# Kernel tuning notes

Measured on AMD Instinct MI355X. Metric: run time of the kernel, lower is better.

The kernel has to match this reference:

```python
import jax, jax.numpy as jnp
import numpy as np

B, n, A = 64, 1024, 32          # graphs, nodes/graph, actions/graph
N = B * n
EH = 2048                        # undirected edges per graph
HID, H = 128, 4
C = HID // H
NF, EF, AD, NI, L = 1, 1, 7, 4, 3
NEG_SLOPE = 0.2


def setup_inputs() -> dict:
    ks = jax.random.split(jax.random.key(0), 16)
    x = jax.random.normal(ks[0], (N, NF), jnp.float32)
    s = jax.random.randint(ks[1], (B, EH), 0, n)
    d = jax.random.randint(ks[2], (B, EH), 0, n)
    off = (jnp.arange(B) * n)[:, None]
    s = (s + off).reshape(-1)
    d = (d + off).reshape(-1)
    # bidirectional edges (unrooted trees): both i->j and j->i
    edge_index = jnp.stack([jnp.concatenate([s, d]), jnp.concatenate([d, s])]).astype(jnp.int32)
    E = edge_index.shape[1]
    edge_attr = jax.random.uniform(ks[3], (E, EF), jnp.float32)
    idx = jax.random.randint(ks[4], (B, A, NI), 0, n).astype(jnp.float32)
    meta = jax.random.normal(ks[5], (B, A, AD - NI), jnp.float32)
    action_tensor = jnp.concatenate([idx, meta], axis=-1)
    batch_idx = jnp.repeat(jnp.arange(B, dtype=jnp.int32), n)
    batch_ptr = jnp.arange(B + 1, dtype=jnp.int32) * n

    def lin(k, i, o):
        return jax.random.normal(k, (i, o), jnp.float32) / np.float32(np.sqrt(i))

    inp = dict(x=x, edge_attr=edge_attr, action_tensor=action_tensor,
               edge_index=edge_index, batch_idx=batch_idx, batch_ptr=batch_ptr)
    inp["Wn"] = lin(ks[6], NF, HID); inp["bn"] = jnp.zeros((HID,), jnp.float32)
    kl = jax.random.split(ks[7], 4 * L)
    inp["gWl"] = jnp.stack([lin(kl[i], HID, HID) for i in range(L)])
    inp["gWr"] = jnp.stack([lin(kl[L + i], HID, HID) for i in range(L)])
    inp["gWe"] = jnp.stack([lin(kl[2 * L + i], EF, HID) for i in range(L)])
    inp["gatt"] = jnp.stack([jax.random.normal(kl[3 * L + i], (H, C), jnp.float32) * 0.1 for i in range(L)])
    inp["gbl"] = jnp.zeros((L, HID), jnp.float32)
    inp["gbr"] = jnp.zeros((L, HID), jnp.float32)
    inp["gb"] = jnp.zeros((L, HID), jnp.float32)
    mlp_in = NI * HID + (AD - NI)
    inp["aW1"] = lin(ks[8], mlp_in, HID); inp["ab1"] = jnp.zeros((HID,), jnp.float32)
    inp["aW2"] = lin(ks[9], HID, HID); inp["ab2"] = jnp.zeros((HID,), jnp.float32)
    inp["qW1"] = lin(ks[10], 4 * HID, HID); inp["qb1"] = jnp.zeros((HID,), jnp.float32)
    inp["qW2"] = lin(ks[11], HID, HID); inp["qb2"] = jnp.zeros((HID,), jnp.float32)
    inp["qW3"] = lin(ks[12], HID, 1); inp["qb3"] = jnp.zeros((1,), jnp.float32)
    return inp


def _gatv2(h, src, dst, ea, Wl, bl, Wr, br, We, att, b):
    # PyG GATv2Conv: e_ij = att . leaky_relu(lin_l(x_j) + lin_r(x_i) + lin_edge(e_ij))
    Nn = h.shape[0]
    xl = (h @ Wl + bl).reshape(Nn, H, C)   # source transform
    xr = (h @ Wr + br).reshape(Nn, H, C)   # target transform
    ee = (ea @ We).reshape(-1, H, C)       # edge transform (no bias in PyG)
    e = jax.nn.leaky_relu(xl[src] + xr[dst] + ee, NEG_SLOPE)   # [E,H,C]
    logits = jnp.einsum('ehc,hc->eh', e, att)
    m = jax.ops.segment_max(logits, dst, num_segments=Nn)       # stable softmax per target node
    ex = jnp.exp(logits - m[dst])
    alpha = ex / jax.ops.segment_sum(ex, dst, num_segments=Nn)[dst]
    msg = (xl[src] * alpha[:, :, None]).reshape(-1, HID)
    return jax.ops.segment_sum(msg, dst, num_segments=Nn) + b


def reference(x, edge_attr, action_tensor, Wn, bn, gWl, gbl, gWr, gbr, gWe, gatt, gb,
              aW1, ab1, aW2, ab2, qW1, qb1, qW2, qb2, qW3, qb3,
              edge_index, batch_idx, batch_ptr):
    Nn = x.shape[0]
    nb = batch_ptr.shape[0] - 1
    # GATv2Conv default add_self_loops=True, fill_value='mean' for edge_attr
    loops = jnp.arange(Nn, dtype=edge_index.dtype)
    src = jnp.concatenate([edge_index[0], loops])
    dst = jnp.concatenate([edge_index[1], loops])
    ea = jnp.concatenate([edge_attr, jnp.broadcast_to(edge_attr.mean(0), (Nn, edge_attr.shape[1]))], 0)
    h = jax.nn.relu(x @ Wn + bn)
    for l in range(L):
        h = jax.nn.relu(_gatv2(h, src, dst, ea, gWl[l], gbl[l], gWr[l], gbr[l], gWe[l], gatt[l], gb[l])) + h
    # sum / mean / max pooling per graph
    sums = jax.ops.segment_sum(h, batch_idx, num_segments=nb)
    cnt = jax.ops.segment_sum(jnp.ones((Nn, 1), h.dtype), batch_idx, num_segments=nb)
    means = sums / cnt
    maxs = jax.ops.segment_max(h, batch_idx, num_segments=nb)
    tree_emb = jnp.concatenate([sums, means, maxs], -1)          # [B, 3*HID]
    # action encoding: gather node embeddings at action node indices (shifted by batch_ptr)
    ni = action_tensor[..., :NI].astype(jnp.int32) + batch_ptr[:-1][:, None, None]
    g = h[ni].reshape(nb, action_tensor.shape[1], NI * HID)
    ai = jnp.concatenate([g, action_tensor[..., NI:]], -1)
    ae = jax.nn.relu(jax.nn.relu(ai @ aW1 + ab1) @ aW2 + ab2)    # [B, A, HID]
    comb = jnp.concatenate([jnp.broadcast_to(tree_emb[:, None, :], (nb, ae.shape[1], 3 * HID)), ae], -1)
    q = jax.nn.relu(comb @ qW1 + qb1)
    q = jax.nn.relu(q @ qW2 + qb2)
    return (q @ qW3 + qb3).squeeze(-1)                            # [B, A]
```

## Files before the change

### kernel.cpp

```cpp
#include <hip/hip_runtime.h>
#include <hip/hip_bf16.h>

#define NNODES 65536
#define NGRAPH 64
#define NPG 1024
#define NACT 32
#define HID 128
#define DEGS 32

typedef __attribute__((ext_vector_type(8))) short bf16x8;
typedef __attribute__((ext_vector_type(4))) float f32x4;

__device__ __forceinline__ void load8(float* dst, const float* src) {
    float4 q0 = ((const float4*)src)[0];
    float4 q1 = ((const float4*)src)[1];
    dst[0]=q0.x; dst[1]=q0.y; dst[2]=q0.z; dst[3]=q0.w;
    dst[4]=q1.x; dst[5]=q1.y; dst[6]=q1.z; dst[7]=q1.w;
}

__device__ __forceinline__ void load8bf(float* dst, const unsigned short* src) {
    uint4 q = *(const uint4*)src;
    dst[0] = __uint_as_float(q.x << 16); dst[1] = __uint_as_float(q.x & 0xffff0000u);
    dst[2] = __uint_as_float(q.y << 16); dst[3] = __uint_as_float(q.y & 0xffff0000u);
    dst[4] = __uint_as_float(q.z << 16); dst[5] = __uint_as_float(q.z & 0xffff0000u);
    dst[6] = __uint_as_float(q.w << 16); dst[7] = __uint_as_float(q.w & 0xffff0000u);
}

__device__ __forceinline__ unsigned short f2bf(float f) {
    unsigned int u = __float_as_uint(f);
    u = (u + 0x7fffu + ((u >> 16) & 1u)) >> 16;
    return (unsigned short)u;
}

__global__ void setup_k(const int* __restrict__ ei, const float* __restrict__ ea,
                        int* __restrict__ cursor, float* __restrict__ meansum,
                        int2* __restrict__ csr, int E0, int nsb,
                        const float* __restrict__ gWl, const float* __restrict__ gWr,
                        unsigned short* __restrict__ wtl, unsigned short* __restrict__ wtr,
                        const float* __restrict__ aW1, const float* __restrict__ aW2,
                        const float* __restrict__ qW1, const float* __restrict__ qW2,
                        unsigned short* __restrict__ wA1t, unsigned short* __restrict__ wA2t,
                        unsigned short* __restrict__ wQ1t, unsigned short* __restrict__ wQ2t) {
    int bid = blockIdx.x, t = threadIdx.x;
    if (bid < nsb) {
        __shared__ float s[256];
        int e = bid * 256 + t;
        float v = 0.f;
        if (e < E0) {
            int sn = ei[e], d = ei[E0 + e];
            int pos = atomicAdd(&cursor[d], 1);
            if (pos >= DEGS) pos = DEGS - 1;
            csr[(size_t)d * DEGS + pos] = make_int2(sn, __float_as_int(ea[e]));
            v = ea[e];
        }
        s[t] = v; __syncthreads();
        for (int off = 128; off > 0; off >>= 1) { if (t < off) s[t] += s[t+off]; __syncthreads(); }
        if (t == 0) atomicAdd(meansum, s[0]);
    } else if (bid < nsb + 192) {
        int idx = (bid - nsb) * 256 + t;
        int l = idx >> 14, rem = idx & 16383;
        int n = rem >> 7, k = rem & 127;
        int src = l*16384 + k*128 + n;
        wtl[idx] = f2bf(gWl[src]);
        wtr[idx] = f2bf(gWr[src]);
    } else {
        int n = bid - nsb - 192;
        for (int k = t; k < 544; k += 256)
            wA1t[n*544 + k] = (k < 515) ? f2bf(aW1[(size_t)k*128 + n]) : (unsigned short)0;
        if (t < 128) {
            wA2t[n*128 + t] = f2bf(aW2[(size_t)t*128 + n]);
            wQ1t[n*128 + t] = f2bf(qW1[(size_t)(384 + t)*128 + n]);
            wQ2t[n*128 + t] = f2bf(qW2[(size_t)t*128 + n]);
        }
    }
}

__global__ __launch_bounds__(256) void gemm_lr_mfma_k(
    const unsigned short* __restrict__ hb, const float* __restrict__ x,
    const float* __restrict__ Wn, const float* __restrict__ bn, int l0,
    const unsigned short* __restrict__ wtl, const unsigned short* __restrict__ wtr,
    const float* __restrict__ bl, const float* __restrict__ br,
    unsigned short* __restrict__ xlb, unsigned short* __restrict__ xrb) {
    int wave = threadIdx.x >> 6;
    int lane = threadIdx.x & 63;
    int lr = lane & 15;
    int lq = lane >> 4;
    int r0 = blockIdx.x * 128 + wave * 32;

    bf16x8 a[2][4];
    if (l0) {
        float xv0 = x[r0 + lr], xv1 = x[r0 + 16 + lr];
#pragma unroll
        for (int kf = 0; kf < 4; ++kf) {
            float wn[8], bv[8];
            load8(wn, Wn + kf*32 + lq*8);
            load8(bv, bn + kf*32 + lq*8);
            union { bf16x8 v; unsigned short u[8]; } p0, p1;
#pragma unroll
            for (int j = 0; j < 8; ++j) {
                p0.u[j] = f2bf(fmaxf(fmaf(xv0, wn[j], bv[j]), 0.f));
                p1.u[j] = f2bf(fmaxf(fmaf(xv1, wn[j], bv[j]), 0.f));
            }
            a[0][kf] = p0.v; a[1][kf] = p1.v;
        }
    } else {
        const short* hs = (const short*)hb;
#pragma unroll
        for (int rt = 0; rt < 2; ++rt)
#pragma unroll
            for (int kf = 0; kf < 4; ++kf)
                a[rt][kf] = *(const bf16x8*)(hs + (size_t)(r0 + rt*16 + lr)*HID + kf*32 + lq*8);
    }

    const short* ws[2]   = {(const short*)wtl, (const short*)wtr};
    const float* bias[2] = {bl, br};
    unsigned short* outp[2] = {xlb, xrb};

#pragma unroll
    for (int m = 0; m < 2; ++m) {
        const short* W = ws[m];
        f32x4 acc[2][8];
#pragma unroll
        for (int rt = 0; rt < 2; ++rt)
#pragma unroll
            for (int ct = 0; ct < 8; ++ct) acc[rt][ct] = (f32x4){0.f,0.f,0.f,0.f};

        bf16x8 b[4], nb2[4];
#pragma unroll
        for (int kf = 0; kf < 4; ++kf)
            b[kf] = *(const bf16x8*)(W + (size_t)(lr)*HID + kf*32 + lq*8);
#pragma unroll
        for (int ct = 0; ct < 8; ++ct) {
            if (ct < 7) {
#pragma unroll
                for (int kf = 0; kf < 4; ++kf)
                    nb2[kf] = *(const bf16x8*)(W + (size_t)((ct+1)*16 + lr)*HID + kf*32 + lq*8);
            }
#pragma unroll
            for (int rt = 0; rt < 2; ++rt)
#pragma unroll
                for (int kf = 0; kf < 4; ++kf)
                    acc[rt][ct] = __builtin_amdgcn_mfma_f32_16x16x32_bf16(a[rt][kf], b[kf], acc[rt][ct], 0, 0, 0);
#pragma unroll
            for (int kf = 0; kf < 4; ++kf) b[kf] = nb2[kf];
        }
#pragma unroll
        for (int ct = 0; ct < 8; ++ct) {
            float bv = bias[m][ct*16 + lr];
#pragma unroll
            for (int rt = 0; rt < 2; ++rt)
#pragma unroll
                for (int rg = 0; rg < 4; ++rg) {
                    int row = r0 + rt*16 + lq*4 + rg;
                    outp[m][(size_t)row*HID + ct*16 + lr] = f2bf(acc[rt][ct][rg] + bv);
                }
        }
    }
}

__global__ __launch_bounds__(256, 4) void gat_edge_k(
    const unsigned short* __restrict__ xlb, const unsigned short* __restrict__ xrb,
    unsigned short* __restrict__ hb,
    const int* __restrict__ deg, const int2* __restrict__ csr,
    const float* __restrict__ We, const float* __restrict__ att,
    const float* __restrict__ gb, const float* __restrict__ meansum, float inv_e0,
    const float* __restrict__ x, const float* __restrict__ Wn, const float* __restrict__ bn,
    int l0, int do_pool, float* __restrict__ tree_sum, float* __restrict__ tree_max) {
    __shared__ float ps[16][132];
    __shared__ float pm[16][132];
    int xcd  = blockIdx.x & 7;
    int slot = blockIdx.x >> 3;
    int g    = xcd * 8 + (slot >> 6);
    int j    = slot & 63;
    int t    = threadIdx.x;
    int nd   = t >> 4;
    int v    = g * NPG + j * 16 + nd;
    int li   = t & 15;
    int base = li * 8;
    float mea = meansum[0] * inv_e0;

    float xrv[8], attv[8], wev[8];
    load8bf(xrv, xrb + (size_t)v*HID + base);
    load8(attv, att + base);
    load8(wev, We + base);

    float acc[8], xs0[8];
    load8bf(xs0, xlb + (size_t)v*HID + base);
    float m;
    {
        float lg = 0.f;
#pragma unroll
        for (int c = 0; c < 8; ++c) {
            float e = xs0[c] + xrv[c] + mea * wev[c];
            e = fmaxf(e, 0.2f * e);
            lg = fmaf(attv[c], e, lg);
        }
        lg += __shfl_xor(lg, 1, 64);
        lg += __shfl_xor(lg, 2, 64);
        m = lg;
#pragma unroll
        for (int c = 0; c < 8; ++c) acc[c] = xs0[c];
    }
    float den = 1.f;

    int dg = deg[v];
    if (dg > DEGS) dg = DEGS;
    const int2* cp = csr + (size_t)v * DEGS;
    for (int i0 = 0; i0 < dg; i0 += 4) {
        int nch = dg - i0; if (nch > 4) nch = 4;
        int2 ee[4];
        float xs[4][8];
#pragma unroll
        for (int u = 0; u < 4; ++u)
            ee[u] = cp[i0 + ((u < nch) ? u : nch - 1)];
#pragma unroll
        for (int u = 0; u < 4; ++u)
            load8bf(xs[u], xlb + (size_t)ee[u].x*HID + base);
#pragma unroll
        for (int u = 0; u < 4; ++u) {
            if (u < nch) {
                float an = __int_as_float(ee[u].y);
                float lg = 0.f;
#pragma unroll
                for (int c = 0; c < 8; ++c) {
                    float e = xs[u][c] + xrv[c] + an * wev[c];
                    e = fmaxf(e, 0.2f * e);
                    lg = fmaf(attv[c], e, lg);
                }
                lg += __shfl_xor(lg, 1, 64);
                lg += __shfl_xor(lg, 2, 64);
                float mn  = fmaxf(m, lg);
                float sc  = __expf(m - mn);
                float wgt = __expf(lg - mn);
                den = den * sc + wgt;
#pragma unroll
                for (int c = 0; c < 8; ++c) acc[c] = acc[c] * sc + wgt * xs[u][c];
                m = mn;
            }
        }
    }

    float inv = 1.f / den;
    size_t o = (size_t)v*HID + base;
    float hold[8], gbv[8];
    if (l0) {
        float xv = x[v];
        float wn[8], bv[8];
        load8(wn, Wn + base);
        load8(bv, bn + base);
#pragma unroll
        for (int c = 0; c < 8; ++c) hold[c] = fmaxf(fmaf(xv, wn[c], bv[c]), 0.f);
    } else {
        load8bf(hold, hb + o);
    }
    load8(gbv, gb + base);
    float nh[8];
#pragma unroll
    for (int c = 0; c < 8; ++c) {
        float val = acc[c] * inv + gbv[c];
        val = val > 0.f ? val : 0.f;
        nh[c] = val + hold[c];
    }
    unsigned int* hbp = (unsigned int*)(hb + o);
#pragma unroll
    for (int q = 0; q < 4; ++q)
        hbp[q] = (unsigned int)f2bf(nh[2*q]) | ((unsigned int)f2bf(nh[2*q+1]) << 16);

    if (do_pool) {
#pragma unroll
        for (int c = 0; c < 8; ++c) { ps[nd][base + c] = nh[c]; pm[nd][base + c] = nh[c]; }
        __syncthreads();
        if (t < 128) {
            float s = 0.f;
#pragma unroll
            for (int n = 0; n < 16; ++n) s += ps[n][t];
            atomicAdd(&tree_sum[g*128 + t], s);
        } else {
            int col = t - 128;
            float mx = 0.f;
#pragma unroll
            for (int n = 0; n < 16; ++n) mx = fmaxf(mx, pm[n][col]);
            atomicMax((int*)&tree_max[g*128 + col], __float_as_int(mx));
        }
    }
}

#define SA1 552
#define SAC 136
__global__ __launch_bounds__(256) void action_q_k(
    const unsigned short* __restrict__ hb, const float* __restrict__ action,
    const int* __restrict__ batch_ptr,
    const float* __restrict__ tree_sum, const float* __restrict__ tree_max,
    const unsigned short* __restrict__ wA1t, const float* __restrict__ ab1,
    const unsigned short* __restrict__ wA2t, const float* __restrict__ ab2,
    const float* __restrict__ qW1, const unsigned short* __restrict__ wQ1t,
    const float* __restrict__ qb1,
    const unsigned short* __restrict__ wQ2t, const float* __restrict__ qb2,
    const float* __restrict__ qW3, const float* __restrict__ qb3,
    float* __restrict__ out) {
    int b = blockIdx.x;
    int t = threadIdx.x;
    int w  = t >> 6;
    int lane = t & 63;
    int lr = lane & 15;
    int lq = lane >> 4;

    __shared__ unsigned short aib[32 * SA1];
    __shared__ unsigned short z1s[32 * SAC];
    __shared__ unsigned short aes[32 * SAC];
    __shared__ unsigned short q1s[32 * SAC];
    __shared__ float q2f[32 * 132];
    __shared__ float tqA[128], tqB[128];
    __shared__ float psum[32][8];

    int ptr = batch_ptr[b];

    {
        int p = t >> 1, half = t & 1;
        int a = p >> 2, j = p & 3;
        const float* actp = action + (size_t)(b * NACT + a) * 7;
        int ni = (int)actp[j] + ptr;
        const uint4* src = (const uint4*)(hb + (size_t)ni * HID) + half * 8;
        uint4* dst = (uint4*)((char*)aib + ((size_t)a * SA1 + j * 128 + half * 64) * 2);
#pragma unroll
        for (int q = 0; q < 8; ++q) dst[q] = src[q];
        if (t < 32) {
            const float* ap = action + (size_t)(b * NACT + t) * 7;
            aib[t * SA1 + 512] = f2bf(ap[4]);
            aib[t * SA1 + 513] = f2bf(ap[5]);
            aib[t * SA1 + 514] = f2bf(ap[6]);
            for (int i = 3; i < 40; ++i) aib[t * SA1 + 512 + i] = 0;
        }
    }

    {
        if (t < 128) {
            int col = t;
            float acc = 0.f;
#pragma unroll 4
            for (int k = 0; k < 128; ++k) {
                float sv = tree_sum[b * 128 + k];
                acc = fmaf(sv, qW1[(size_t)k * 128 + col], acc);
                acc = fmaf(sv * (1.f / 1024.f), qW1[(size_t)(128 + k) * 128 + col], acc);
            }
            tqA[col] = acc;
        } else {
            int col = t - 128;
            float acc = 0.f;
#pragma unroll 4
            for (int k = 0; k < 128; ++k) {
                float mv = tree_max[b * 128 + k];
                acc = fmaf(mv, qW1[(size_t)(256 + k) * 128 + col], acc);
            }
            tqB[col] = acc;
        }
    }
    __syncthreads();

    f32x4 acc[2][2];
    const unsigned short* srcA;
    int strideA, K;

    srcA = aib; strideA = SA1; K = 544;
#pragma unroll
    for (int rt = 0; rt < 2; ++rt)
#pragma unroll
        for (int ci = 0; ci < 2; ++ci) acc[rt][ci] = (f32x4){0.f, 0.f, 0.f, 0.f};
    for (int ks = 0; ks < K; ks += 32) {
        bf16x8 a0 = *(const bf16x8*)(srcA + (0 * 16 + lr) * strideA + ks + lq * 8);
        bf16x8 a1 = *(const bf16x8*)(srcA + (1 * 16 + lr) * strideA + ks + lq * 8);
        bf16x8 b0 = *(const bf16x8*)(wA1t + (size_t)((2 * w + 0) * 16 + lr) * K + ks + lq * 8);
        bf16x8 b1 = *(const bf16x8*)(wA1t + (size_t)((2 * w + 1) * 16 + lr) * K + ks + lq * 8);
        acc[0][0] = __builtin_amdgcn_mfma_f32_16x16x32_bf16(a0, b0, acc[0][0], 0, 0, 0);
        acc[0][1] = __builtin_amdgcn_mfma_f32_16x16x32_bf16(a0, b1, acc[0][1], 0, 0, 0);
        acc[1][0] = __builtin_amdgcn_mfma_f32_16x16x32_bf16(a1, b0, acc[1][0], 0, 0, 0);
        acc[1][1] = __builtin_amdgcn_mfma_f32_16x16x32_bf16(a1, b1, acc[1][1], 0, 0, 0);
    }
#pragma unroll
    for (int ci = 0; ci < 2; ++ci) {
        int col = (2 * w + ci) * 16 + lr;
        float bv = ab1[col];
#pragma unroll
        for (int rt = 0; rt < 2; ++rt)
#pragma unroll
            for (int rg = 0; rg < 4; ++rg) {
                int row = rt * 16 + lq * 4 + rg;
                z1s[row * SAC + col] = f2bf(fmaxf(acc[rt][ci][rg] + bv, 0.f));
            }
    }
    __syncthreads();

    srcA = z1s; strideA = SAC; K = 128;
#pragma unroll
    for (int rt = 0; rt < 2; ++rt)
#pragma unroll
        for (int ci = 0; ci < 2; ++ci) acc[rt][ci] = (f32x4){0.f, 0.f, 0.f, 0.f};
#pragma unroll
    for (int ks = 0; ks < 128; ks += 32) {
        bf16x8 a0 = *(const bf16x8*)(srcA + (0 * 16 + lr) * strideA + ks + lq * 8);
        bf16x8 a1 = *(const bf16x8*)(srcA + (1 * 16 + lr) * strideA + ks + lq * 8);
        bf16x8 b0 = *(const bf16x8*)(wA2t + (size_t)((2 * w + 0) * 16 + lr) * K + ks + lq * 8);
        bf16x8 b1 = *(const bf16x8*)(wA2t + (size_t)((2 * w + 1) * 16 + lr) * K + ks + lq * 8);
        acc[0][0] = __builtin_amdgcn_mfma_f32_16x16x32_bf16(a0, b0, acc[0][0], 0, 0, 0);
        acc[0][1] = __builtin_amdgcn_mfma_f32_16x16x32_bf16(a0, b1, acc[0][1], 0, 0, 0);
        acc[1][0] = __builtin_amdgcn_mfma_f32_16x16x32_bf16(a1, b0, acc[1][0], 0, 0, 0);
        acc[1][1] = __builtin_amdgcn_mfma_f32_16x16x32_bf16(a1, b1, acc[1][1], 0, 0, 0);
    }
#pragma unroll
    for (int ci = 0; ci < 2; ++ci) {
        int col = (2 * w + ci) * 16 + lr;
        float bv = ab2[col];
#pragma unroll
        for (int rt = 0; rt < 2; ++rt)
#pragma unroll
            for (int rg = 0; rg < 4; ++rg) {
                int row = rt * 16 + lq * 4 + rg;
                aes[row * SAC + col] = f2bf(fmaxf(acc[rt][ci][rg] + bv, 0.f));
            }
    }
    __syncthreads();

    srcA = aes; strideA = SAC; K = 128;
#pragma unroll
    for (int rt = 0; rt < 2; ++rt)
#pragma unroll
        for (int ci = 0; ci < 2; ++ci) acc[rt][ci] = (f32x4){0.f, 0.f, 0.f, 0.f};
#pragma unroll
    for (int ks = 0; ks < 128; ks += 32) {
        bf16x8 a0 = *(const bf16x8*)(srcA + (0 * 16 + lr) * strideA + ks + lq * 8);
        bf16x8 a1 = *(const bf16x8*)(srcA + (1 * 16 + lr) * strideA + ks + lq * 8);
        bf16x8 b0 = *(const bf16x8*)(wQ1t + (size_t)((2 * w + 0) * 16 + lr) * K + ks + lq * 8);
        bf16x8 b1 = *(const bf16x8*)(wQ1t + (size_t)((2 * w + 1) * 16 + lr) * K + ks + lq * 8);
        acc[0][0] = __builtin_amdgcn_mfma_f32_16x16x32_bf16(a0, b0, acc[0][0], 0, 0, 0);
        acc[0][1] = __builtin_amdgcn_mfma_f32_16x16x32_bf16(a0, b1, acc[0][1], 0, 0, 0);
        acc[1][0] = __builtin_amdgcn_mfma_f32_16x16x32_bf16(a1, b0, acc[1][0], 0, 0, 0);
        acc[1][1] = __builtin_amdgcn_mfma_f32_16x16x32_bf16(a1, b1, acc[1][1], 0, 0, 0);
    }
#pragma unroll
    for (int ci = 0; ci < 2; ++ci) {
        int col = (2 * w + ci) * 16 + lr;
        float bv = qb1[col] + tqA[col] + tqB[col];
#pragma unroll
        for (int rt = 0; rt < 2; ++rt)
#pragma unroll
            for (int rg = 0; rg < 4; ++rg) {
                int row = rt * 16 + lq * 4 + rg;
                q1s[row * SAC + col] = f2bf(fmaxf(acc[rt][ci][rg] + bv, 0.f));
            }
    }
    __syncthreads();

    srcA = q1s; strideA = SAC; K = 128;
#pragma unroll
    for (int rt = 0; rt < 2; ++rt)
#pragma unroll
        for (int ci = 0; ci < 2; ++ci) acc[rt][ci] = (f32x4){0.f, 0.f, 0.f, 0.f};
#pragma unroll
    for (int ks = 0; ks < 128; ks += 32) {
        bf16x8 a0 = *(const bf16x8*)(srcA + (0 * 16 + lr) * strideA + ks + lq * 8);
        bf16x8 a1 = *(const bf16x8*)(srcA + (1 * 16 + lr) * strideA + ks + lq * 8);
        bf16x8 b0 = *(const bf16x8*)(wQ2t + (size_t)((2 * w + 0) * 16 + lr) * K + ks + lq * 8);
        bf16x8 b1 = *(const bf16x8*)(wQ2t + (size_t)((2 * w + 1) * 16 + lr) * K + ks + lq * 8);
        acc[0][0] = __builtin_amdgcn_mfma_f32_16x16x32_bf16(a0, b0, acc[0][0], 0, 0, 0);
        acc[0][1] = __builtin_amdgcn_mfma_f32_16x16x32_bf16(a0, b1, acc[0][1], 0, 0, 0);
        acc[1][0] = __builtin_amdgcn_mfma_f32_16x16x32_bf16(a1, b0, acc[1][0], 0, 0, 0);
        acc[1][1] = __builtin_amdgcn_mfma_f32_16x16x32_bf16(a1, b1, acc[1][1], 0, 0, 0);
    }
#pragma unroll
    for (int ci = 0; ci < 2; ++ci) {
        int col = (2 * w + ci) * 16 + lr;
        float bv = qb2[col];
#pragma unroll
        for (int rt = 0; rt < 2; ++rt)
#pragma unroll
            for (int rg = 0; rg < 4; ++rg) {
                int row = rt * 16 + lq * 4 + rg;
                q2f[row * 132 + col] = fmaxf(acc[rt][ci][rg] + bv, 0.f);
            }
    }
    __syncthreads();

    {
        int a = t >> 3, seg = t & 7;
        float s = 0.f;
#pragma unroll
        for (int k = 0; k < 16; ++k)
            s = fmaf(q2f[a * 132 + seg * 16 + k], qW3[seg * 16 + k], s);
        psum[a][seg] = s;
    }
    __syncthreads();
    if (t < 32) {
        float s = qb3[0];
#pragma unroll
        for (int i = 0; i < 8; ++i) s += psum[t][i];
        out[(size_t)b * NACT + t] = s;
    }
}

extern "C" void kernel_launch(void* const* d_in, const int* in_sizes, int n_in,
                              void* d_out, int out_size, void* d_ws, size_t ws_size,
                              hipStream_t stream) {
    const float* x         = (const float*)d_in[0];
    const float* edge_attr = (const float*)d_in[1];
    const float* action    = (const float*)d_in[2];
    const int*   edge_idx  = (const int*)d_in[3];
    const int*   batch_ptr = (const int*)d_in[5];
    const float* Wn  = (const float*)d_in[6];
    const float* bn  = (const float*)d_in[7];
    const float* gWl = (const float*)d_in[8];
    const float* gWr = (const float*)d_in[9];
    const float* gWe = (const float*)d_in[10];
    const float* gatt= (const float*)d_in[11];
    const float* gbl = (const float*)d_in[12];
    const float* gbr = (const float*)d_in[13];
    const float* gb  = (const float*)d_in[14];
    const float* aW1 = (const float*)d_in[15];
    const float* ab1 = (const float*)d_in[16];
    const float* aW2 = (const float*)d_in[17];
    const float* ab2 = (const float*)d_in[18];
    const float* qW1 = (const float*)d_in[19];
    const float* qb1 = (const float*)d_in[20];
    const float* qW2 = (const float*)d_in[21];
    const float* qb2 = (const float*)d_in[22];
    const float* qW3 = (const float*)d_in[23];
    const float* qb3 = (const float*)d_in[24];
    float* out = (float*)d_out;

    const int E0 = in_sizes[1];
    const int N  = NNODES;

    char* w = (char*)d_ws;
    auto alloc = [&](size_t bytes) { void* p = (void*)w; w += (bytes + 255) & ~(size_t)255; return p; };
    unsigned short* hb  = (unsigned short*)alloc((size_t)N * HID * 2);
    unsigned short* xlb = (unsigned short*)alloc((size_t)N * HID * 2);
    unsigned short* xrb = (unsigned short*)alloc((size_t)N * HID * 2);
    int2*  csr      = (int2*)alloc((size_t)N * DEGS * 8);
    int*   cursor   = (int*)alloc((size_t)N * 4);
    float* meansum  = (float*)alloc(256);
    float* tree_sum = (float*)alloc((size_t)NGRAPH * 128 * 4);
    float* tree_max = (float*)alloc((size_t)NGRAPH * 128 * 4);
    size_t zero_span = (size_t)((char*)(tree_max + NGRAPH * 128) - (char*)cursor);
    unsigned short* wtl = (unsigned short*)alloc((size_t)3*128*128*2);
    unsigned short* wtr = (unsigned short*)alloc((size_t)3*128*128*2);
    unsigned short* wA1t = (unsigned short*)alloc((size_t)128*544*2);
    unsigned short* wA2t = (unsigned short*)alloc((size_t)128*128*2);
    unsigned short* wQ1t = (unsigned short*)alloc((size_t)128*128*2);
    unsigned short* wQ2t = (unsigned short*)alloc((size_t)128*128*2);

    hipMemsetAsync(cursor, 0, zero_span, stream);

    int nsb = (E0 + 255) / 256;
    setup_k<<<nsb + 320, 256, 0, stream>>>(edge_idx, edge_attr, cursor, meansum, csr, E0, nsb,
                                           gWl, gWr, wtl, wtr,
                                           aW1, aW2, qW1, qW2, wA1t, wA2t, wQ1t, wQ2t);

    float inv_e0 = 1.0f / (float)E0;
    for (int l = 0; l < 3; ++l) {
        gemm_lr_mfma_k<<<N / 128, 256, 0, stream>>>(
            hb, x, Wn, bn, (l == 0) ? 1 : 0,
            wtl + (size_t)l*128*128, wtr + (size_t)l*128*128,
            gbl + l*HID, gbr + l*HID, xlb, xrb);
        gat_edge_k<<<N / 16, 256, 0, stream>>>(
            xlb, xrb, hb, cursor, csr,
            gWe + l*HID, gatt + l*128, gb + l*HID, meansum, inv_e0,
            x, Wn, bn, (l == 0) ? 1 : 0, (l == 2) ? 1 : 0, tree_sum, tree_max);
    }

    action_q_k<<<NGRAPH, 256, 0, stream>>>(
        hb, action, batch_ptr, tree_sum, tree_max,
        wA1t, ab1, wA2t, ab2, qW1, wQ1t, qb1, wQ2t, qb2, qW3, qb3, out);
}
```

Baseline: 304.6 us.

## Fuse next-layer Wl/Wr GEMM into GAT edge aggregation kernel

The GAT aggregation kernel for layers 0 and 1 now stages each block's 16 new node rows in shared memory and immediately computes the next layer's left/right projections with MFMA. This removes two separate GEMM launches and the global re-read of h between layers. Ping-pong xl/xr buffers avoid read-write hazards. The cost is reloading the full weight matrices per 16-row block (from L2) and lower MFMA efficiency per block.

Result: slower. 312.8 us (+2.7%).

```diff
diff --git a/kernel.cpp b/kernel.cpp
--- a/kernel.cpp
+++ b/kernel.cpp
@@ -7,6 +7,7 @@
 #define NACT 32
 #define HID 128
 #define DEGS 32
+#define SAC 136
 
 typedef __attribute__((ext_vector_type(8))) short bf16x8;
 typedef __attribute__((ext_vector_type(4))) float f32x4;
@@ -17,7 +18,6 @@
     dst[0]=q0.x; dst[1]=q0.y; dst[2]=q0.z; dst[3]=q0.w;
     dst[4]=q1.x; dst[5]=q1.y; dst[6]=q1.z; dst[7]=q1.w;
 }
-
 __device__ __forceinline__ void load8bf(float* dst, const unsigned short* src) {
     uint4 q = *(const uint4*)src;
     dst[0] = __uint_as_float(q.x << 16); dst[1] = __uint_as_float(q.x & 0xffff0000u);
@@ -25,7 +25,6 @@
     dst[4] = __uint_as_float(q.z << 16); dst[5] = __uint_as_float(q.z & 0xffff0000u);
     dst[6] = __uint_as_float(q.w << 16); dst[7] = __uint_as_float(q.w & 0xffff0000u);
 }
-
 __device__ __forceinline__ unsigned short f2bf(float f) {
     unsigned int u = __float_as_uint(f);
     u = (u + 0x7fffu + ((u >> 16) & 1u)) >> 16;
@@ -75,47 +74,34 @@
     }
 }
 
-__global__ __launch_bounds__(256) void gemm_lr_mfma_k(
-    const unsigned short* __restrict__ hb, const float* __restrict__ x,
-    const float* __restrict__ Wn, const float* __restrict__ bn, int l0,
+__global__ __launch_bounds__(256) void gemm0_k(
+    const float* __restrict__ x, const float* __restrict__ Wn, const float* __restrict__ bn,
     const unsigned short* __restrict__ wtl, const unsigned short* __restrict__ wtr,
     const float* __restrict__ bl, const float* __restrict__ br,
     unsigned short* __restrict__ xlb, unsigned short* __restrict__ xrb) {
-    int wave = threadIdx.x >> 6;
-    int lane = threadIdx.x & 63;
-    int lr = lane & 15;
-    int lq = lane >> 4;
+    int wave = threadIdx.x >> 6, lane = threadIdx.x & 63;
+    int lr = lane & 15, lq = lane >> 4;
     int r0 = blockIdx.x * 128 + wave * 32;
 
     bf16x8 a[2][4];
-    if (l0) {
-        float xv0 = x[r0 + lr], xv1 = x[r0 + 16 + lr];
-#pragma unroll
-        for (int kf = 0; kf < 4; ++kf) {
-            float wn[8], bv[8];
-            load8(wn, Wn + kf*32 + lq*8);
-            load8(bv, bn + kf*32 + lq*8);
-            union { bf16x8 v; unsigned short u[8]; } p0, p1;
-#pragma unroll
-            for (int j = 0; j < 8; ++j) {
-                p0.u[j] = f2bf(fmaxf(fmaf(xv0, wn[j], bv[j]), 0.f));
-                p1.u[j] = f2bf(fmaxf(fmaf(xv1, wn[j], bv[j]), 0.f));
-            }
-            a[0][kf] = p0.v; a[1][kf] = p1.v;
-        }
-    } else {
-        const short* hs = (const short*)hb;
-#pragma unroll
-        for (int rt = 0; rt < 2; ++rt)
-#pragma unroll
-            for (int kf = 0; kf < 4; ++kf)
-                a[rt][kf] = *(const bf16x8*)(hs + (size_t)(r0 + rt*16 + lr)*HID + kf*32 + lq*8);
+    float xv0 = x[r0 + lr], xv1 = x[r0 + 16 + lr];
+#pragma unroll
+    for (int kf = 0; kf < 4; ++kf) {
+        float wn[8], bv[8];
+        load8(wn, Wn + kf*32 + lq*8);
+        load8(bv, bn + kf*32 + lq*8);
+        union { bf16x8 v; unsigned short u[8]; } p0, p1;
+#pragma unroll
+        for (int j = 0; j < 8; ++j) {
+            p0.u[j] = f2bf(fmaxf(fmaf(xv0, wn[j], bv[j]), 0.f));
+            p1.u[j] = f2bf(fmaxf(fmaf(xv1, wn[j], bv[j]), 0.f));
+        }
+        a[0][kf] = p0.v; a[1][kf] = p1.v;
     }
 
     const short* ws[2]   = {(const short*)wtl, (const short*)wtr};
     const float* bias[2] = {bl, br};
     unsigned short* outp[2] = {xlb, xrb};
-
 #pragma unroll
     for (int m = 0; m < 2; ++m) {
         const short* W = ws[m];
@@ -124,11 +110,10 @@
         for (int rt = 0; rt < 2; ++rt)
 #pragma unroll
             for (int ct = 0; ct < 8; ++ct) acc[rt][ct] = (f32x4){0.f,0.f,0.f,0.f};
-
         bf16x8 b[4], nb2[4];
 #pragma unroll
         for (int kf = 0; kf < 4; ++kf)
-            b[kf] = *(const bf16x8*)(W + (size_t)(lr)*HID + kf*32 + lq*8);
+            b[kf] = *(const bf16x8*)(W + (size_t)lr*HID + kf*32 + lq*8);
 #pragma unroll
         for (int ct = 0; ct < 8; ++ct) {
             if (ct < 7) {
@@ -150,10 +135,159 @@
 #pragma unroll
             for (int rt = 0; rt < 2; ++rt)
 #pragma unroll
-                for (int rg = 0; rg < 4; ++rg) {
-                    int row = r0 + rt*16 + lq*4 + rg;
-                    outp[m][(size_t)row*HID + ct*16 + lr] = f2bf(acc[rt][ct][rg] + bv);
+                for (int rg = 0; rg < 4; ++rg)
+                    outp[m][(size_t)(r0 + rt*16 + lq*4 + rg)*HID + ct*16 + lr] = f2bf(acc[rt][ct][rg] + bv);
+        }
+    }
+}
+
+__global__ __launch_bounds__(256, 4) void gatgemm_k(
+    const unsigned short* __restrict__ xli, const unsigned short* __restrict__ xri,
+    unsigned short* __restrict__ hb,
+    const int* __restrict__ deg, const int2* __restrict__ csr,
+    const float* __restrict__ We, const float* __restrict__ att,
+    const float* __restrict__ gb, const float* __restrict__ meansum, float inv_e0,
+    const float* __restrict__ x, const float* __restrict__ Wn, const float* __restrict__ bn, int l0,
+    const unsigned short* __restrict__ wtlN, const unsigned short* __restrict__ wtrN,
+    const float* __restrict__ blN, const float* __restrict__ brN,
+    unsigned short* __restrict__ xlo, unsigned short* __restrict__ xro) {
+    __shared__ unsigned short sA[16 * SAC];
+    int xcd  = blockIdx.x & 7;
+    int slot = blockIdx.x >> 3;
+    int g    = xcd * 8 + (slot >> 6);
+    int j    = slot & 63;
+    int t    = threadIdx.x;
+    int nd   = t >> 4;
+    int vb   = g * NPG + j * 16;
+    int v    = vb + nd;
+    int li   = t & 15;
+    int base = li * 8;
+    float mea = meansum[0] * inv_e0;
+
+    float xrv[8], attv[8], wev[8];
+    load8bf(xrv, xri + (size_t)v*HID + base);
+    load8(attv, att + base);
+    load8(wev, We + base);
+
+    float acc[8], xs0[8];
+    load8bf(xs0, xli + (size_t)v*HID + base);
+    float m;
+    {
+        float lg = 0.f;
+#pragma unroll
+        for (int c = 0; c < 8; ++c) {
+            float e = xs0[c] + xrv[c] + mea * wev[c];
+            e = fmaxf(e, 0.2f * e);
+            lg = fmaf(attv[c], e, lg);
+        }
+        lg += __shfl_xor(lg, 1, 64);
+        lg += __shfl_xor(lg, 2, 64);
+        m = lg;
+#pragma unroll
+        for (int c = 0; c < 8; ++c) acc[c] = xs0[c];
+    }
+    float den = 1.f;
+
+    int dg = deg[v];
+    if (dg > DEGS) dg = DEGS;
+    const int2* cp = csr + (size_t)v * DEGS;
+    for (int i0 = 0; i0 < dg; i0 += 4) {
+        int nch = dg - i0; if (nch > 4) nch = 4;
+        int2 ee[4];
+        float xs[4][8];
+#pragma unroll
+        for (int u = 0; u < 4; ++u)
+            ee[u] = cp[i0 + ((u < nch) ? u : nch - 1)];
+#pragma unroll
+        for (int u = 0; u < 4; ++u)
+            load8bf(xs[u], xli + (size_t)ee[u].x*HID + base);
+#pragma unroll
+        for (int u = 0; u < 4; ++u) {
+            if (u < nch) {
+                float an = __int_as_float(ee[u].y);
+                float lg = 0.f;
+#pragma unroll
+                for (int c = 0; c < 8; ++c) {
+                    float e = xs[u][c] + xrv[c] + an * wev[c];
+                    e = fmaxf(e, 0.2f * e);
+                    lg = fmaf(attv[c], e, lg);
                 }
+                lg += __shfl_xor(lg, 1, 64);
+                lg += __shfl_xor(lg, 2, 64);
+                float mn  = fmaxf(m, lg);
+                float sc  = __expf(m - mn);
+                float wgt = __expf(lg - mn);
+                den = den * sc + wgt;
+#pragma unroll
+                for (int c = 0; c < 8; ++c) acc[c] = acc[c] * sc + wgt * xs[u][c];
+                m = mn;
+            }
+        }
+    }
+
+    float inv = 1.f / den;
+    size_t o = (size_t)v*HID + base;
+    float hold[8], gbv[8];
+    if (l0) {
+        float xv = x[v];
+        float wn[8], bv[8];
+        load8(wn, Wn + base);
+        load8(bv, bn + base);
+#pragma unroll
+        for (int c = 0; c < 8; ++c) hold[c] = fmaxf(fmaf(xv, wn[c], bv[c]), 0.f);
+    } else {
+        load8bf(hold, hb + o);
+    }
+    load8(gbv, gb + base);
+    float nh[8];
+#pragma unroll
+    for (int c = 0; c < 8; ++c) {
+        float val = acc[c] * inv + gbv[c];
+        val = val > 0.f ? val : 0.f;
+        nh[c] = val + hold[c];
+    }
+    unsigned int pk[4];
+#pragma unroll
+    for (int q = 0; q < 4; ++q)
+        pk[q] = (unsigned int)f2bf(nh[2*q]) | ((unsigned int)f2bf(nh[2*q+1]) << 16);
+    unsigned int* hbp = (unsigned int*)(hb + o);
+#pragma unroll
+    for (int q = 0; q < 4; ++q) hbp[q] = pk[q];
+    unsigned int* sAp = (unsigned int*)(sA + nd * SAC + base);
+#pragma unroll
+    for (int q = 0; q < 4; ++q) sAp[q] = pk[q];
+    __syncthreads();
+
+    int wave = t >> 6, lane = t & 63, lr = lane & 15, lq = lane >> 4;
+    bf16x8 afr[4];
+#pragma unroll
+    for (int kf = 0; kf < 4; ++kf)
+        afr[kf] = *(const bf16x8*)(sA + lr * SAC + kf*32 + lq*8);
+    const short* ws[2]   = {(const short*)wtlN, (const short*)wtrN};
+    const float* bias[2] = {blN, brN};
+    unsigned short* outp[2] = {xlo, xro};
+#pragma unroll
+    for (int mm = 0; mm < 2; ++mm) {
+        const short* W = ws[mm];
+        f32x4 gac[2];
+#pragma unroll
+        for (int ci = 0; ci < 2; ++ci) gac[ci] = (f32x4){0.f,0.f,0.f,0.f};
+#pragma unroll
+        for (int ci = 0; ci < 2; ++ci) {
+            int ct = wave * 2 + ci;
+#pragma unroll
+            for (int kf = 0; kf < 4; ++kf) {
+                bf16x8 bv = *(const bf16x8*)(W + (size_t)(ct*16 + lr)*HID + kf*32 + lq*8);
+                gac[ci] = __builtin_amdgcn_mfma_f32_16x16x32_bf16(afr[kf], bv, gac[ci], 0, 0, 0);
+            }
+        }
+#pragma unroll
+        for (int ci = 0; ci < 2; ++ci) {
+            int ct = wave * 2 + ci;
+            float bv = bias[mm][ct*16 + lr];
+#pragma unroll
+            for (int rg = 0; rg < 4; ++rg)
+                outp[mm][(size_t)(vb + lq*4 + rg)*HID + ct*16 + lr] = f2bf(gac[ci][rg] + bv);
         }
     }
 }
@@ -164,8 +298,7 @@
     const int* __restrict__ deg, const int2* __restrict__ csr,
     const float* __restrict__ We, const float* __restrict__ att,
     const float* __restrict__ gb, const float* __restrict__ meansum, float inv_e0,
-    const float* __restrict__ x, const float* __restrict__ Wn, const float* __restrict__ bn,
-    int l0, int do_pool, float* __restrict__ tree_sum, float* __restrict__ tree_max) {
+    float* __restrict__ tree_sum, float* __restrict__ tree_max) {
     __shared__ float ps[16][132];
     __shared__ float pm[16][132];
     int xcd  = blockIdx.x & 7;
@@ -243,16 +376,7 @@
     float inv = 1.f / den;
     size_t o = (size_t)v*HID + base;
     float hold[8], gbv[8];
-    if (l0) {
-        float xv = x[v];
-        float wn[8], bv[8];
-        load8(wn, Wn + base);
-        load8(bv, bn + base);
-#pragma unroll
-        for (int c = 0; c < 8; ++c) hold[c] = fmaxf(fmaf(xv, wn[c], bv[c]), 0.f);
-    } else {
-        load8bf(hold, hb + o);
-    }
+    load8bf(hold, hb + o);
     load8(gbv, gb + base);
     float nh[8];
 #pragma unroll
@@ -266,27 +390,24 @@
     for (int q = 0; q < 4; ++q)
         hbp[q] = (unsigned int)f2bf(nh[2*q]) | ((unsigned int)f2bf(nh[2*q+1]) << 16);
 
-    if (do_pool) {
-#pragma unroll
-        for (int c = 0; c < 8; ++c) { ps[nd][base + c] = nh[c]; pm[nd][base + c] = nh[c]; }
-        __syncthreads();
-        if (t < 128) {
-            float s = 0.f;
-#pragma unroll
-            for (int n = 0; n < 16; ++n) s += ps[n][t];
-            atomicAdd(&tree_sum[g*128 + t], s);
-        } else {
-            int col = t - 128;
-            float mx = 0.f;
-#pragma unroll
-            for (int n = 0; n < 16; ++n) mx = fmaxf(mx, pm[n][col]);
-            atomicMax((int*)&tree_max[g*128 + col], __float_as_int(mx));
-        }
+#pragma unroll
+    for (int c = 0; c < 8; ++c) { ps[nd][base + c] = nh[c]; pm[nd][base + c] = nh[c]; }
+    __syncthreads();
+    if (t < 128) {
+        float s = 0.f;
+#pragma unroll
+        for (int n = 0; n < 16; ++n) s += ps[n][t];
+        atomicAdd(&tree_sum[g*128 + t], s);
+    } else {
+        int col = t - 128;
+        float mx = 0.f;
+#pragma unroll
+        for (int n = 0; n < 16; ++n) mx = fmaxf(mx, pm[n][col]);
+        atomicMax((int*)&tree_max[g*128 + col], __float_as_int(mx));
     }
 }
 
 #define SA1 552
-#define SAC 136
 __global__ __launch_bounds__(256) void action_q_k(
     const unsigned short* __restrict__ hb, const float* __restrict__ action,
     const int* __restrict__ batch_ptr,
@@ -532,16 +653,18 @@
     char* w = (char*)d_ws;
     auto alloc = [&](size_t bytes) { void* p = (void*)w; w += (bytes + 255) & ~(size_t)255; return p; };
     unsigned short* hb  = (unsigned short*)alloc((size_t)N * HID * 2);
-    unsigned short* xlb = (unsigned short*)alloc((size_t)N * HID * 2);
-    unsigned short* xrb = (unsigned short*)alloc((size_t)N * HID * 2);
+    unsigned short* xl0 = (unsigned short*)alloc((size_t)N * HID * 2);
+    unsigned short* xr0 = (unsigned short*)alloc((size_t)N * HID * 2);
+    unsigned short* xl1 = (unsigned short*)alloc((size_t)N * HID * 2);
+    unsigned short* xr1 = (unsigned short*)alloc((size_t)N * HID * 2);
     int2*  csr      = (int2*)alloc((size_t)N * DEGS * 8);
     int*   cursor   = (int*)alloc((size_t)N * 4);
     float* meansum  = (float*)alloc(256);
     float* tree_sum = (float*)alloc((size_t)NGRAPH * 128 * 4);
     float* tree_max = (float*)alloc((size_t)NGRAPH * 128 * 4);
     size_t zero_span = (size_t)((char*)(tree_max + NGRAPH * 128) - (char*)cursor);
-    unsigned short* wtl = (unsigned short*)alloc((size_t)3*128*128*2);
-    unsigned short* wtr = (unsigned short*)alloc((size_t)3*128*128*2);
+    unsigned short* wtl  = (unsigned short*)alloc((size_t)3*128*128*2);
+    unsigned short* wtr  = (unsigned short*)alloc((size_t)3*128*128*2);
     unsigned short* wA1t = (unsigned short*)alloc((size_t)128*544*2);
     unsigned short* wA2t = (unsigned short*)alloc((size_t)128*128*2);
     unsigned short* wQ1t = (unsigned short*)alloc((size_t)128*128*2);
@@ -555,16 +678,23 @@
                                            aW1, aW2, qW1, qW2, wA1t, wA2t, wQ1t, wQ2t);
 
     float inv_e0 = 1.0f / (float)E0;
-    for (int l = 0; l < 3; ++l) {
-        gemm_lr_mfma_k<<<N / 128, 256, 0, stream>>>(
-            hb, x, Wn, bn, (l == 0) ? 1 : 0,
-            wtl + (size_t)l*128*128, wtr + (size_t)l*128*128,
-            gbl + l*HID, gbr + l*HID, xlb, xrb);
-        gat_edge_k<<<N / 16, 256, 0, stream>>>(
-            xlb, xrb, hb, cursor, csr,
-            gWe + l*HID, gatt + l*128, gb + l*HID, meansum, inv_e0,
-            x, Wn, bn, (l == 0) ? 1 : 0, (l == 2) ? 1 : 0, tree_sum, tree_max);
-    }
+    gemm0_k<<<N / 128, 256, 0, stream>>>(x, Wn, bn, wtl, wtr, gbl, gbr, xl0, xr0);
+    gatgemm_k<<<N / 16, 256, 0, stream>>>(
+        xl0, xr0, hb, cursor, csr,
+        gWe + 0*HID, gatt + 0*128, gb + 0*HID, meansum, inv_e0,
+        x, Wn, bn, 1,
+        wtl + (size_t)1*16384, wtr + (size_t)1*16384, gbl + 1*HID, gbr + 1*HID,
+        xl1, xr1);
+    gatgemm_k<<<N / 16, 256, 0, stream>>>(
+        xl1, xr1, hb, cursor, csr,
+        gWe + 1*HID, gatt + 1*128, gb + 1*HID, meansum, inv_e0,
+        x, Wn, bn, 0,
+        wtl + (size_t)2*16384, wtr + (size_t)2*16384, gbl + 2*HID, gbr + 2*HID,
+        xl0, xr0);
+    gat_edge_k<<<N / 16, 256, 0, stream>>>(
+        xl0, xr0, hb, cursor, csr,
+        gWe + 2*HID, gatt + 2*128, gb + 2*HID, meansum, inv_e0,
+        tree_sum, tree_max);
 
     action_q_k<<<NGRAPH, 256, 0, stream>>>(
         hb, action, batch_ptr, tree_sum, tree_max,
```
